# Kernel tuning notes

Hardware: AMD Instinct MI355X
Metric: run time of the kernel (lower is better)

## Reference

```python
import jax, jax.numpy as jnp
import numpy as np

BATCH = 65536
VOCAB = 1048576
EMBED = 128
N_DENSE = 13
N_SPARSE = 26
BOT_DIMS = (512, 256, 128)
TOP_DIMS = (1024, 1024, 512, 256, 1)
TOP_IN = 506  # 128 + 27*28/2


def setup_inputs() -> dict:
    key = jax.random.key(0)
    ks = jax.random.split(key, 32)
    inp = {}
    inp['dense'] = jax.random.normal(ks[0], (BATCH, N_DENSE), dtype=jnp.float32)
    inp['sparse_idx'] = jax.random.randint(ks[1], (BATCH, N_SPARSE), 0, VOCAB, dtype=jnp.int32)
    # embedding table (concatenation of the 4 chunks is mathematically one table)
    scale = 1.0 / np.sqrt(VOCAB)
    inp['emb'] = scale * jax.random.uniform(ks[2], (VOCAB, EMBED), dtype=jnp.float32)
    # bottom MLP params
    fan_in = N_DENSE
    ki = 3
    for i, d in enumerate(BOT_DIMS):
        limit = np.sqrt(6.0 / (fan_in + d))
        inp[f'bw{i}'] = jax.random.uniform(ks[ki], (fan_in, d), jnp.float32, -limit, limit); ki += 1
        inp[f'bb{i}'] = np.sqrt(1.0 / d) * jax.random.normal(ks[ki], (d,), jnp.float32); ki += 1
        fan_in = d
    # top MLP params
    fan_in = TOP_IN
    for i, d in enumerate(TOP_DIMS):
        inp[f'tw{i}'] = np.sqrt(2.0 / (fan_in + d)) * jax.random.normal(ks[ki], (fan_in, d), jnp.float32); ki += 1
        inp[f'tb{i}'] = np.sqrt(1.0 / d) * jax.random.normal(ks[ki], (d,), jnp.float32); ki += 1
        fan_in = d
    return inp


def _triu_idx():
    r, c = np.triu_indices(N_SPARSE + 1)  # includes diagonal, matches torch.triu_indices
    return jnp.asarray(r), jnp.asarray(c)


def reference(dense, sparse_idx, emb,
              bw0, bb0, bw1, bb1, bw2, bb2,
              tw0, tb0, tw1, tb1, tw2, tb2, tw3, tb3, tw4, tb4):
    # bottom MLP
    h = dense
    for w, b in ((bw0, bb0), (bw1, bb1), (bw2, bb2)):
        h = jax.nn.relu(h @ w + b)
    # embedding lookup (modulo as in original)
    idx = jnp.mod(sparse_idx, VOCAB)
    emb_sparse = emb[idx.reshape(-1)].reshape(dense.shape[0], N_SPARSE, EMBED)
    # dot interaction
    combined = jnp.concatenate([h[:, None, :], emb_sparse], axis=1)  # [B, 27, 128]
    inter = jnp.einsum('bnd,bmd->bnm', combined, combined)           # [B, 27, 27]
    r, c = _triu_idx()
    inter_flat = inter[:, r, c]                                      # [B, 378]
    top = jnp.concatenate([h, inter_flat], axis=1)                   # [B, 506]
    # top MLP (ReLU on all but last layer)
    tws = (tw0, tw1, tw2, tw3, tw4)
    tbs = (tb0, tb1, tb2, tb3, tb4)
    for i in range(len(tws)):
        top = top @ tws[i] + tbs[i]
        if i < len(tws) - 1:
            top = jax.nn.relu(top)
    return top  # [B, 1]
```

## Files before the change

kernel.cpp:

```cpp
#include <hip/hip_runtime.h>

#define BATCH 65536
#define NSP 26
#define NROW 27
#define VOCAB_MASK (1048576 - 1)

typedef unsigned short u16;
typedef unsigned int u32;
typedef float f32x4 __attribute__((ext_vector_type(4)));
typedef float f32x16 __attribute__((ext_vector_type(16)));
typedef __bf16 bf16x8 __attribute__((ext_vector_type(8)));

__device__ __forceinline__ u16 f2bf(float f) {
    u32 u = __float_as_uint(f);
    u = (u + 0x7FFFu + ((u >> 16) & 1u)) >> 16;
    return (u16)u;
}
__device__ __forceinline__ float bf2f(u16 h) { return __uint_as_float(((u32)h) << 16); }
__device__ __forceinline__ void fsplit(float x, u16& hi, u16& lo) {
    hi = f2bf(x);
    lo = f2bf(x - bf2f(hi));
}
__device__ __forceinline__ __bf16 u2b(u16 h) { union { u16 u; __bf16 b; } c; c.u = h; return c.b; }

#define GLD16(gp, lp) __builtin_amdgcn_global_load_lds( \
    (const __attribute__((address_space(1))) u32*)(gp), \
    (__attribute__((address_space(3))) u32*)(lp), 16, 0, 0)

__global__ __launch_bounds__(256) void gemm_mfma(
    const u16* __restrict__ Ahi, const u16* __restrict__ Alo,
    const u16* __restrict__ Whi, const u16* __restrict__ Wlo,
    const float* __restrict__ bias,
    u16* __restrict__ Chi, u16* __restrict__ Clo,
    int M, int K, int N, int relu)
{
    __shared__ u16 sAh[4096], sAl[4096], sWh[4096], sWl[4096];
    const int tid = threadIdx.x;
    const int w = tid >> 6, lane = tid & 63;
    const int wr = w >> 1, wc = w & 1;
    const int m0 = blockIdx.y * 128, n0 = blockIdx.x * 128;
    const int ml = lane & 15, q = lane >> 4;

    f32x4 acc[4][4];
#pragma unroll
    for (int i = 0; i < 4; ++i)
#pragma unroll
        for (int j = 0; j < 4; ++j)
#pragma unroll
            for (int r = 0; r < 4; ++r) acc[i][j][r] = 0.f;

    const int nIter = K >> 5;
    for (int it = 0; it < nIter; ++it) {
        const int c = it * 4 + w;
#pragma unroll
        for (int h = 0; h < 2; ++h) {
            const size_t ga = ((size_t)c * M + m0 + h * 64 + lane) * 8;
            const size_t gw = ((size_t)c * N + n0 + h * 64 + lane) * 8;
            GLD16(Ahi + ga, sAh + w * 1024 + h * 512);
            GLD16(Alo + ga, sAl + w * 1024 + h * 512);
            GLD16(Whi + gw, sWh + w * 1024 + h * 512);
            GLD16(Wlo + gw, sWl + w * 1024 + h * 512);
        }
        __syncthreads();

        const int ab = q * 1024 + wr * 512 + ml * 8;
        const int bb = q * 1024 + wc * 512 + ml * 8;
        bf16x8 ah[4], al[4], bh[4], bl[4];
#pragma unroll
        for (int t = 0; t < 4; ++t) {
            ah[t] = *(const bf16x8*)&sAh[ab + t * 128];
            al[t] = *(const bf16x8*)&sAl[ab + t * 128];
            bh[t] = *(const bf16x8*)&sWh[bb + t * 128];
            bl[t] = *(const bf16x8*)&sWl[bb + t * 128];
        }
#pragma unroll
        for (int i = 0; i < 4; ++i)
#pragma unroll
            for (int j = 0; j < 4; ++j) {
                f32x4 a = acc[i][j];
                a = __builtin_amdgcn_mfma_f32_16x16x32_bf16(al[i], bh[j], a, 0, 0, 0);
                a = __builtin_amdgcn_mfma_f32_16x16x32_bf16(ah[i], bl[j], a, 0, 0, 0);
                a = __builtin_amdgcn_mfma_f32_16x16x32_bf16(ah[i], bh[j], a, 0, 0, 0);
                acc[i][j] = a;
            }
        __syncthreads();
    }

#pragma unroll
    for (int j = 0; j < 4; ++j) {
        const int n = n0 + wc * 64 + j * 16 + ml;
        const float bs = bias[n];
        const size_t cb = (size_t)(n >> 3) * M * 8 + (n & 7);
#pragma unroll
        for (int i = 0; i < 4; ++i) {
            const int mbase = m0 + wr * 64 + i * 16 + q * 4;
#pragma unroll
            for (int r = 0; r < 4; ++r) {
                float x = acc[i][j][r] + bs;
                if (relu) x = fmaxf(x, 0.f);
                u16 hi, lo; fsplit(x, hi, lo);
                const size_t off = cb + (size_t)(mbase + r) * 8;
                Chi[off] = hi; Clo[off] = lo;
            }
        }
    }
}

__global__ void conv_w(const float* __restrict__ W, u16* __restrict__ Whi,
                       u16* __restrict__ Wlo, int Kreal, int Kpad, int N)
{
    const int idx = blockIdx.x * 256 + threadIdx.x;
    if (idx >= (Kpad >> 3) * N) return;
    const int c = idx / N, n = idx - c * N;
#pragma unroll
    for (int j = 0; j < 8; ++j) {
        const int k = c * 8 + j;
        const float x = (k < Kreal) ? W[(size_t)k * N + n] : 0.f;
        u16 hi, lo; fsplit(x, hi, lo);
        Whi[(size_t)idx * 8 + j] = hi;
        Wlo[(size_t)idx * 8 + j] = lo;
    }
}

__global__ void conv_dense(const float* __restrict__ dense,
                           u16* __restrict__ Dhi, u16* __restrict__ Dlo)
{
    const int m = blockIdx.x * 256 + threadIdx.x;
    float v[13];
#pragma unroll
    for (int j = 0; j < 13; ++j) v[j] = dense[(size_t)m * 13 + j];
#pragma unroll
    for (int cc = 0; cc < 4; ++cc) {
        const size_t base = ((size_t)cc * BATCH + m) * 8;
#pragma unroll
        for (int j = 0; j < 8; ++j) {
            const int k = cc * 8 + j;
            const float x = (k < 13) ? v[k] : 0.f;
            u16 hi, lo; fsplit(x, hi, lo);
            Dhi[base + j] = hi; Dlo[base + j] = lo;
        }
    }
}

__global__ __launch_bounds__(256) void interact_kernel(
    u16* __restrict__ Xhi, u16* __restrict__ Xlo,
    const int* __restrict__ sidx, const float* __restrict__ emb)
{
    const int wave = threadIdx.x >> 6, lane = threadIdx.x & 63;
    const int b = blockIdx.x * 4 + wave;
    const int r = lane & 31, half = lane >> 5;

    bf16x8 fh[8], fl[8];

    if (r == 0) {
#pragma unroll
        for (int s = 0; s < 8; ++s) {
            const size_t base = ((size_t)(2 * s + half) * BATCH + b) * 8;
            fh[s] = *(const bf16x8*)&Xhi[base];
            fl[s] = *(const bf16x8*)&Xlo[base];
        }
    } else if (r <= NSP) {
        const int ix = sidx[(size_t)b * NSP + (r - 1)] & VOCAB_MASK;
        const float* ep = emb + (size_t)ix * 128 + half * 8;
        float4 v[8][2];
#pragma unroll
        for (int s = 0; s < 8; ++s) {
            v[s][0] = *(const float4*)(ep + s * 16);
            v[s][1] = *(const float4*)(ep + s * 16 + 4);
        }
#pragma unroll
        for (int s = 0; s < 8; ++s) {
            const float f[8] = {v[s][0].x, v[s][0].y, v[s][0].z, v[s][0].w,
                                v[s][1].x, v[s][1].y, v[s][1].z, v[s][1].w};
#pragma unroll
            for (int j = 0; j < 8; ++j) {
                u16 hi, lo; fsplit(f[j], hi, lo);
                fh[s][j] = u2b(hi); fl[s][j] = u2b(lo);
            }
        }
    } else {
#pragma unroll
        for (int s = 0; s < 8; ++s) {
#pragma unroll
            for (int j = 0; j < 8; ++j) { fh[s][j] = u2b(0); fl[s][j] = u2b(0); }
        }
    }

    f32x16 acc = {};
#pragma unroll
    for (int s = 0; s < 8; ++s) {
        acc = __builtin_amdgcn_mfma_f32_32x32x16_bf16(fl[s], fh[s], acc, 0, 0, 0);
        acc = __builtin_amdgcn_mfma_f32_32x32x16_bf16(fh[s], fl[s], acc, 0, 0, 0);
        acc = __builtin_amdgcn_mfma_f32_32x32x16_bf16(fh[s], fh[s], acc, 0, 0, 0);
    }

    const int col = lane & 31;
    if (col < NROW) {
#pragma unroll
        for (int reg = 0; reg < 16; ++reg) {
            const int row = (reg & 3) + 8 * (reg >> 2) + 4 * half;
            if (row > col) continue;
            const int k = 128 + row * NROW - (row * (row - 1)) / 2 - row + col;
            u16 hi, lo; fsplit(acc[reg], hi, lo);
            const size_t off = ((size_t)(k >> 3) * BATCH + b) * 8 + (k & 7);
            Xhi[off] = hi; Xlo[off] = lo;
        }
    }
    if (lane < 6) {
        const int k = 506 + lane;
        const size_t off = ((size_t)(k >> 3) * BATCH + b) * 8 + (k & 7);
        Xhi[off] = 0; Xlo[off] = 0;
    }
}

__global__ __launch_bounds__(256) void final_dot(
    const u16* __restrict__ Ahi, const u16* __restrict__ Alo,
    const float* __restrict__ wv, const float* __restrict__ bias,
    float* __restrict__ out)
{
    const int wave = threadIdx.x >> 6, lane = threadIdx.x & 63;
    const int b = blockIdx.x * 4 + wave;
    const int c = lane & 31;
    const u16* src = (lane >= 32) ? Alo : Ahi;
    const size_t base = ((size_t)c * BATCH + b) * 8;
    float s = 0.f;
#pragma unroll
    for (int j = 0; j < 8; ++j) s += bf2f(src[base + j]) * wv[c * 8 + j];
#pragma unroll
    for (int off = 32; off > 0; off >>= 1) s += __shfl_down(s, off);
    if (lane == 0) out[b] = s + bias[0];
}

extern "C" void kernel_launch(void* const* d_in, const int* in_sizes, int n_in,
                              void* d_out, int out_size, void* d_ws, size_t ws_size,
                              hipStream_t stream)
{
    const float* dense = (const float*)d_in[0];
    const int*   sidx  = (const int*)d_in[1];
    const float* emb   = (const float*)d_in[2];
    const float* bw0 = (const float*)d_in[3],  *bb0 = (const float*)d_in[4];
    const float* bw1 = (const float*)d_in[5],  *bb1 = (const float*)d_in[6];
    const float* bw2 = (const float*)d_in[7],  *bb2 = (const float*)d_in[8];
    const float* tw0 = (const float*)d_in[9],  *tb0 = (const float*)d_in[10];
    const float* tw1 = (const float*)d_in[11], *tb1 = (const float*)d_in[12];
    const float* tw2 = (const float*)d_in[13], *tb2 = (const float*)d_in[14];
    const float* tw3 = (const float*)d_in[15], *tb3 = (const float*)d_in[16];
    const float* tw4 = (const float*)d_in[17], *tb4 = (const float*)d_in[18];
    float* out = (float*)d_out;

    char* p = (char*)d_ws;
    const size_t ACT = (size_t)BATCH * 1024 * sizeof(u16);
    u16* Xhi = (u16*)p; p += ACT;
    u16* Xlo = (u16*)p; p += ACT;
    u16* Yhi = (u16*)p; p += ACT;
    u16* Ylo = (u16*)p; p += ACT;
    u16* D0hi = (u16*)p; p += (size_t)BATCH * 32 * sizeof(u16);
    u16* D0lo = (u16*)p; p += (size_t)BATCH * 32 * sizeof(u16);
    auto alloc_w = [&](size_t elems, u16** hi, u16** lo) {
        *hi = (u16*)p; p += elems * sizeof(u16);
        *lo = (u16*)p; p += elems * sizeof(u16);
    };
    u16 *W0h,*W0l,*W1h,*W1l,*W2h,*W2l,*T0h,*T0l,*T1h,*T1l,*T2h,*T2l,*T3h,*T3l;
    alloc_w(32 * 512, &W0h, &W0l);
    alloc_w(512 * 256, &W1h, &W1l);
    alloc_w(256 * 128, &W2h, &W2l);
    alloc_w(512 * 1024, &T0h, &T0l);
    alloc_w(1024 * 1024, &T1h, &T1l);
    alloc_w(1024 * 512, &T2h, &T2l);
    alloc_w(512 * 256, &T3h, &T3l);

    const dim3 blk(256);
    auto cwg = [](int kpad, int n) { return dim3(((kpad >> 3) * n + 255) / 256); };

    conv_dense<<<BATCH / 256, blk, 0, stream>>>(dense, D0hi, D0lo);
    conv_w<<<cwg(32, 512),    blk, 0, stream>>>(bw0, W0h, W0l, 13,   32,   512);
    conv_w<<<cwg(512, 256),   blk, 0, stream>>>(bw1, W1h, W1l, 512,  512,  256);
    conv_w<<<cwg(256, 128),   blk, 0, stream>>>(bw2, W2h, W2l, 256,  256,  128);
    conv_w<<<cwg(512, 1024),  blk, 0, stream>>>(tw0, T0h, T0l, 506,  512,  1024);
    conv_w<<<cwg(1024, 1024), blk, 0, stream>>>(tw1, T1h, T1l, 1024, 1024, 1024);
    conv_w<<<cwg(1024, 512),  blk, 0, stream>>>(tw2, T2h, T2l, 1024, 1024, 512);
    conv_w<<<cwg(512, 256),   blk, 0, stream>>>(tw3, T3h, T3l, 512,  512,  256);

    gemm_mfma<<<dim3(4, 512), blk, 0, stream>>>(D0hi, D0lo, W0h, W0l, bb0, Xhi, Xlo, BATCH, 32,  512, 1);
    gemm_mfma<<<dim3(2, 512), blk, 0, stream>>>(Xhi, Xlo, W1h, W1l, bb1, Yhi, Ylo, BATCH, 512, 256, 1);
    gemm_mfma<<<dim3(1, 512), blk, 0, stream>>>(Yhi, Ylo, W2h, W2l, bb2, Xhi, Xlo, BATCH, 256, 128, 1);

    interact_kernel<<<dim3(BATCH / 4), blk, 0, stream>>>(Xhi, Xlo, sidx, emb);

    gemm_mfma<<<dim3(8, 512), blk, 0, stream>>>(Xhi, Xlo, T0h, T0l, tb0, Yhi, Ylo, BATCH, 512,  1024, 1);
    gemm_mfma<<<dim3(8, 512), blk, 0, stream>>>(Yhi, Ylo, T1h, T1l, tb1, Xhi, Xlo, BATCH, 1024, 1024, 1);
    gemm_mfma<<<dim3(4, 512), blk, 0, stream>>>(Xhi, Xlo, T2h, T2l, tb2, Yhi, Ylo, BATCH, 1024, 512,  1);
    gemm_mfma<<<dim3(2, 512), blk, 0, stream>>>(Yhi, Ylo, T3h, T3l, tb3, Xhi, Xlo, BATCH, 512,  256,  1);
    final_dot<<<dim3(BATCH / 4), blk, 0, stream>>>(Xhi, Xlo, tw4, tb4, out);
}
```

Measured before the change: 2.235 ms.

## Restructure split-bf16 GEMM with 256x128 tiles, triple-buffered LDS, 32x32 MFMA

The GEMM kernel now uses 512-thread blocks computing 256x128 output tiles. MFMA moves from 16x16x32 to 32x32x16, and the K loop is software-pipelined over a three-stage LDS ring using async global-to-LDS loads with explicit vmcnt waits and raw barriers. A workgroup index remap groups neighbouring tiles for L2 reuse. The aim is to hide global load latency behind the MFMA work and to raise arithmetic intensity per LDS read. In exchange it uses 144KB of LDS per block, which lowers occupancy, and the hand-written waitcnt/barrier sync is fragile.

```diff
diff --git a/kernel.cpp b/kernel.cpp
--- a/kernel.cpp
+++ b/kernel.cpp
@@ -27,79 +27,121 @@
     (const __attribute__((address_space(1))) u32*)(gp), \
     (__attribute__((address_space(3))) u32*)(lp), 16, 0, 0)
 
-__global__ __launch_bounds__(256) void gemm_mfma(
+__global__ __launch_bounds__(512, 2) void gemm_mfma(
     const u16* __restrict__ Ahi, const u16* __restrict__ Alo,
     const u16* __restrict__ Whi, const u16* __restrict__ Wlo,
     const float* __restrict__ bias,
     u16* __restrict__ Chi, u16* __restrict__ Clo,
     int M, int K, int N, int relu)
 {
-    __shared__ u16 sAh[4096], sAl[4096], sWh[4096], sWl[4096];
+    __shared__ __align__(16) u16 sbuf[3][24576];
+
     const int tid = threadIdx.x;
     const int w = tid >> 6, lane = tid & 63;
     const int wr = w >> 1, wc = w & 1;
-    const int m0 = blockIdx.y * 128, n0 = blockIdx.x * 128;
-    const int ml = lane & 15, q = lane >> 4;
-
-    f32x4 acc[4][4];
-#pragma unroll
-    for (int i = 0; i < 4; ++i)
-#pragma unroll
-        for (int j = 0; j < 4; ++j)
-#pragma unroll
-            for (int r = 0; r < 4; ++r) acc[i][j][r] = 0.f;
-
-    const int nIter = K >> 5;
-    for (int it = 0; it < nIter; ++it) {
-        const int c = it * 4 + w;
-#pragma unroll
-        for (int h = 0; h < 2; ++h) {
-            const size_t ga = ((size_t)c * M + m0 + h * 64 + lane) * 8;
-            const size_t gw = ((size_t)c * N + n0 + h * 64 + lane) * 8;
-            GLD16(Ahi + ga, sAh + w * 1024 + h * 512);
-            GLD16(Alo + ga, sAl + w * 1024 + h * 512);
-            GLD16(Whi + gw, sWh + w * 1024 + h * 512);
-            GLD16(Wlo + gw, sWl + w * 1024 + h * 512);
-        }
-        __syncthreads();
-
-        const int ab = q * 1024 + wr * 512 + ml * 8;
-        const int bb = q * 1024 + wc * 512 + ml * 8;
-        bf16x8 ah[4], al[4], bh[4], bl[4];
-#pragma unroll
-        for (int t = 0; t < 4; ++t) {
-            ah[t] = *(const bf16x8*)&sAh[ab + t * 128];
-            al[t] = *(const bf16x8*)&sAl[ab + t * 128];
-            bh[t] = *(const bf16x8*)&sWh[bb + t * 128];
-            bl[t] = *(const bf16x8*)&sWl[bb + t * 128];
-        }
-#pragma unroll
-        for (int i = 0; i < 4; ++i)
-#pragma unroll
-            for (int j = 0; j < 4; ++j) {
-                f32x4 a = acc[i][j];
-                a = __builtin_amdgcn_mfma_f32_16x16x32_bf16(al[i], bh[j], a, 0, 0, 0);
-                a = __builtin_amdgcn_mfma_f32_16x16x32_bf16(ah[i], bl[j], a, 0, 0, 0);
-                a = __builtin_amdgcn_mfma_f32_16x16x32_bf16(ah[i], bh[j], a, 0, 0, 0);
-                acc[i][j] = a;
+    const int rl = lane & 31, hl = lane >> 5;
+
+    const int d = blockIdx.y * gridDim.x + blockIdx.x;
+    const int nwg = gridDim.x * gridDim.y;
+    const int wg = (d & 7) * (nwg >> 3) + (d >> 3);
+    const int bx = wg % gridDim.x, by = wg / gridDim.x;
+    const int m0 = by * 256, n0 = bx * 128;
+
+    const int nT = K >> 5;
+
+    const u16* gp[6];
+    int loff[6], gstr[6];
+#pragma unroll
+    for (int s = 0; s < 6; ++s) {
+        const int u = w * 6 + s;
+        if (u < 32) {
+            const int uu = u & 15, c = uu >> 2, gq = uu & 3;
+            gp[s] = ((u < 16) ? Ahi : Alo) + ((size_t)c * M + m0 + gq * 64 + lane) * 8;
+            loff[s] = ((u < 16) ? 0 : 8192) + c * 2048 + gq * 512;
+            gstr[s] = M * 32;
+        } else {
+            const int uu = u & 7, c = uu >> 1, gq = uu & 1;
+            gp[s] = ((u < 40) ? Whi : Wlo) + ((size_t)c * N + n0 + gq * 64 + lane) * 8;
+            loff[s] = ((u < 40) ? 16384 : 20480) + c * 1024 + gq * 512;
+            gstr[s] = N * 32;
+        }
+    }
+    auto stage = [&](int buf) {
+        u16* lb = &sbuf[buf][0];
+#pragma unroll
+        for (int s = 0; s < 6; ++s) {
+            GLD16(gp[s], lb + loff[s]);
+            gp[s] += gstr[s];
+        }
+    };
+
+    f32x16 acc[2][2];
+#pragma unroll
+    for (int i = 0; i < 2; ++i)
+#pragma unroll
+        for (int j = 0; j < 2; ++j)
+#pragma unroll
+            for (int r = 0; r < 16; ++r) acc[i][j][r] = 0.f;
+
+    stage(0);
+    if (nT > 1) stage(1);
+
+    int bufC = 0;
+    for (int t = 0; t < nT; ++t) {
+        if (t + 2 < nT) {
+            stage((bufC == 0) ? 2 : bufC - 1);
+            asm volatile("s_waitcnt vmcnt(12)" ::: "memory");
+        } else if (t + 1 < nT) {
+            asm volatile("s_waitcnt vmcnt(6)" ::: "memory");
+        } else {
+            asm volatile("s_waitcnt vmcnt(0)" ::: "memory");
+        }
+        asm volatile("s_barrier" ::: "memory");
+
+        const u16* sb = sbuf[bufC];
+#pragma unroll
+        for (int ks = 0; ks < 2; ++ks) {
+            const int c = ks * 2 + hl;
+            bf16x8 ah[2], al[2], bh[2], blo[2];
+#pragma unroll
+            for (int i = 0; i < 2; ++i) {
+                const int ra = wr * 64 + i * 32 + rl;
+                ah[i]  = *(const bf16x8*)&sb[c * 2048 + ra * 8];
+                al[i]  = *(const bf16x8*)&sb[8192 + c * 2048 + ra * 8];
+                const int rb = wc * 64 + i * 32 + rl;
+                bh[i]  = *(const bf16x8*)&sb[16384 + c * 1024 + rb * 8];
+                blo[i] = *(const bf16x8*)&sb[20480 + c * 1024 + rb * 8];
             }
-        __syncthreads();
-    }
-
-#pragma unroll
-    for (int j = 0; j < 4; ++j) {
-        const int n = n0 + wc * 64 + j * 16 + ml;
+#pragma unroll
+            for (int i = 0; i < 2; ++i)
+#pragma unroll
+                for (int j = 0; j < 2; ++j) {
+                    f32x16 a = acc[i][j];
+                    a = __builtin_amdgcn_mfma_f32_32x32x16_bf16(al[i], bh[j],  a, 0, 0, 0);
+                    a = __builtin_amdgcn_mfma_f32_32x32x16_bf16(ah[i], blo[j], a, 0, 0, 0);
+                    a = __builtin_amdgcn_mfma_f32_32x32x16_bf16(ah[i], bh[j],  a, 0, 0, 0);
+                    acc[i][j] = a;
+                }
+        }
+        asm volatile("s_barrier" ::: "memory");
+        bufC = (bufC == 2) ? 0 : bufC + 1;
+    }
+
+#pragma unroll
+    for (int j = 0; j < 2; ++j) {
+        const int n = n0 + wc * 64 + j * 32 + rl;
         const float bs = bias[n];
         const size_t cb = (size_t)(n >> 3) * M * 8 + (n & 7);
 #pragma unroll
-        for (int i = 0; i < 4; ++i) {
-            const int mbase = m0 + wr * 64 + i * 16 + q * 4;
-#pragma unroll
-            for (int r = 0; r < 4; ++r) {
-                float x = acc[i][j][r] + bs;
+        for (int i = 0; i < 2; ++i) {
+            const int mb = m0 + wr * 64 + i * 32 + 4 * hl;
+#pragma unroll
+            for (int reg = 0; reg < 16; ++reg) {
+                const int row = (reg & 3) + 8 * (reg >> 2);
+                float x = acc[i][j][reg] + bs;
                 if (relu) x = fmaxf(x, 0.f);
                 u16 hi, lo; fsplit(x, hi, lo);
-                const size_t off = cb + (size_t)(mbase + r) * 8;
+                const size_t off = cb + (size_t)(mb + row) * 8;
                 Chi[off] = hi; Clo[off] = lo;
             }
         }
@@ -270,6 +312,7 @@
     alloc_w(512 * 256, &T3h, &T3l);
 
     const dim3 blk(256);
+    const dim3 gblk(512);
     auto cwg = [](int kpad, int n) { return dim3(((kpad >> 3) * n + 255) / 256); };
 
     conv_dense<<<BATCH / 256, blk, 0, stream>>>(dense, D0hi, D0lo);
@@ -281,15 +324,15 @@
     conv_w<<<cwg(1024, 512),  blk, 0, stream>>>(tw2, T2h, T2l, 1024, 1024, 512);
     conv_w<<<cwg(512, 256),   blk, 0, stream>>>(tw3, T3h, T3l, 512,  512,  256);
 
-    gemm_mfma<<<dim3(4, 512), blk, 0, stream>>>(D0hi, D0lo, W0h, W0l, bb0, Xhi, Xlo, BATCH, 32,  512, 1);
-    gemm_mfma<<<dim3(2, 512), blk, 0, stream>>>(Xhi, Xlo, W1h, W1l, bb1, Yhi, Ylo, BATCH, 512, 256, 1);
-    gemm_mfma<<<dim3(1, 512), blk, 0, stream>>>(Yhi, Ylo, W2h, W2l, bb2, Xhi, Xlo, BATCH, 256, 128, 1);
+    gemm_mfma<<<dim3(4, 256), gblk, 0, stream>>>(D0hi, D0lo, W0h, W0l, bb0, Xhi, Xlo, BATCH, 32,  512, 1);
+    gemm_mfma<<<dim3(2, 256), gblk, 0, stream>>>(Xhi, Xlo, W1h, W1l, bb1, Yhi, Ylo, BATCH, 512, 256, 1);
+    gemm_mfma<<<dim3(1, 256), gblk, 0, stream>>>(Yhi, Ylo, W2h, W2l, bb2, Xhi, Xlo, BATCH, 256, 128, 1);
 
     interact_kernel<<<dim3(BATCH / 4), blk, 0, stream>>>(Xhi, Xlo, sidx, emb);
 
-    gemm_mfma<<<dim3(8, 512), blk, 0, stream>>>(Xhi, Xlo, T0h, T0l, tb0, Yhi, Ylo, BATCH, 512,  1024, 1);
-    gemm_mfma<<<dim3(8, 512), blk, 0, stream>>>(Yhi, Ylo, T1h, T1l, tb1, Xhi, Xlo, BATCH, 1024, 1024, 1);
-    gemm_mfma<<<dim3(4, 512), blk, 0, stream>>>(Xhi, Xlo, T2h, T2l, tb2, Yhi, Ylo, BATCH, 1024, 512,  1);
-    gemm_mfma<<<dim3(2, 512), blk, 0, stream>>>(Yhi, Ylo, T3h, T3l, tb3, Xhi, Xlo, BATCH, 512,  256,  1);
+    gemm_mfma<<<dim3(8, 256), gblk, 0, stream>>>(Xhi, Xlo, T0h, T0l, tb0, Yhi, Ylo, BATCH, 512,  1024, 1);
+    gemm_mfma<<<dim3(8, 256), gblk, 0, stream>>>(Yhi, Ylo, T1h, T1l, tb1, Xhi, Xlo, BATCH, 1024, 1024, 1);
+    gemm_mfma<<<dim3(4, 256), gblk, 0, stream>>>(Xhi, Xlo, T2h, T2l, tb2, Yhi, Ylo, BATCH, 1024, 512,  1);
+    gemm_mfma<<<dim3(2, 256), gblk, 0, stream>>>(Yhi, Ylo, T3h, T3l, tb3, Xhi, Xlo, BATCH, 512,  256,  1);
     final_dot<<<dim3(BATCH / 4), blk, 0, stream>>>(Xhi, Xlo, tw4, tb4, out);
 }
```

Result: faster. 2.097 ms (-6.2%).
